# Kernel tuning notes

Hardware: AMD Instinct MI355X
Metric: run time of the kernel (lower is better)

Reference implementation:

```python
import jax, jax.numpy as jnp
import numpy as np

QUERY_DIM = 512
KEY_DIM = 512
HIDDEN_DIM = 512


def setup_inputs() -> dict:
    key = jax.random.key(0)
    k1, k2, k3, k4, k5 = jax.random.split(key, 5)
    B, S = 32, 2048
    query = jax.random.normal(k1, (B, QUERY_DIM), dtype=jnp.float32)
    keys = jax.random.normal(k2, (B, S, KEY_DIM), dtype=jnp.float32)
    # nn.Linear weights stored as [out_features, in_features]
    Wq = jax.random.normal(k3, (HIDDEN_DIM, QUERY_DIM), dtype=jnp.float32) / np.sqrt(QUERY_DIM)
    Wk = jax.random.normal(k4, (HIDDEN_DIM, KEY_DIM), dtype=jnp.float32) / np.sqrt(KEY_DIM)
    w_att = jax.random.normal(k5, (HIDDEN_DIM,), dtype=jnp.float32) / np.sqrt(HIDDEN_DIM)
    return {"query": query, "keys": keys, "Wq": Wq, "Wk": Wk, "w_att": w_att}


def reference(query, keys, Wq, Wk, w_att):
    # values defaults to keys
    values = keys
    q = query @ Wq.T                               # [B, H]
    k = jnp.einsum('bsd,hd->bsh', keys, Wk)        # [B, S, H]
    combined = jnp.tanh(q[:, None, :] + k)         # [B, S, H]
    scores = jnp.einsum('bsh,h->bs', combined, w_att)  # [B, S]
    attn = jax.nn.softmax(scores, axis=-1)         # [B, S]
    out = jnp.einsum('bs,bsd->bd', attn, values)   # [B, D]
    return (out, attn)
```

## Files before the change

kernel.cpp:

```cpp
#include <hip/hip_runtime.h>
#include <hip/hip_fp16.h>

typedef _Float16 f16x8 __attribute__((ext_vector_type(8)));
typedef float f32x4 __attribute__((ext_vector_type(4)));

#define WS_QV 0
#define WS_BF 65536
#define WS_SC 589824
#define WS_VP 851968

__global__ __launch_bounds__(256) void prep_kernel(
    const float* __restrict__ query, const float* __restrict__ Wq,
    const float* __restrict__ Wk, float* __restrict__ qv,
    _Float16* __restrict__ bfrag) {
  const int blk = blockIdx.x, tid = threadIdx.x;
  if (blk < 64) {
    const int b = blk >> 1;
    const int h = ((blk & 1) << 8) + tid;
    const float4* qr = (const float4*)(query + (size_t)b * 512);
    const float4* wr = (const float4*)(Wq + (size_t)h * 512);
    float acc = 0.f;
#pragma unroll 8
    for (int i = 0; i < 128; ++i) {
      float4 a = qr[i], w = wr[i];
      acc += a.x * w.x + a.y * w.y + a.z * w.z + a.w * w.w;
    }
    qv[b * 512 + h] = acc;
  } else {
    const int u = (blk - 64) * 4 + (tid >> 6);
    const int l = tid & 63;
    const int col = ((u >> 4) << 4) + (l & 15);
    const int k0 = ((u & 15) << 5) + ((l >> 4) << 3);
    const float4* src = (const float4*)(Wk + (size_t)col * 512 + k0);
    float4 x = src[0], y = src[1];
    f16x8 v;
    v[0] = (_Float16)x.x; v[1] = (_Float16)x.y;
    v[2] = (_Float16)x.z; v[3] = (_Float16)x.w;
    v[4] = (_Float16)y.x; v[5] = (_Float16)y.y;
    v[6] = (_Float16)y.z; v[7] = (_Float16)y.w;
    *(f16x8*)(bfrag + (size_t)u * 512 + l * 8) = v;
  }
}

__global__ __launch_bounds__(256, 2) void scores_kernel(
    const float* __restrict__ keys, const _Float16* __restrict__ bfrag,
    const float* __restrict__ qv, const float* __restrict__ w_att,
    float* __restrict__ scores) {
  __shared__ __align__(128) unsigned char lds[65536];
  const int tid = threadIdx.x, w = tid >> 6, l = tid & 63;
  const int wg = blockIdx.x;
  const int row0 = wg * 64;
  const int b = row0 >> 11;

  {
    const float* kb = keys + (size_t)row0 * 512;
#pragma unroll
    for (int j = 0; j < 16; ++j) {
      int u8 = j * 256 + tid;
      int r = u8 >> 6, c8 = u8 & 63;
      const float4* src = (const float4*)(kb + (size_t)r * 512 + c8 * 8);
      float4 x = src[0], y = src[1];
      f16x8 v;
      v[0] = (_Float16)x.x; v[1] = (_Float16)x.y;
      v[2] = (_Float16)x.z; v[3] = (_Float16)x.w;
      v[4] = (_Float16)y.x; v[5] = (_Float16)y.y;
      v[6] = (_Float16)y.z; v[7] = (_Float16)y.w;
      int byte = r * 1024 + c8 * 16;
      byte ^= (r & 7) << 4;
      *(f16x8*)(lds + byte) = v;
    }
  }
  __syncthreads();

  f32x4 acc[4][8];
#pragma unroll
  for (int mt = 0; mt < 4; ++mt)
#pragma unroll
    for (int nt = 0; nt < 8; ++nt) {
      acc[mt][nt][0] = 0.f; acc[mt][nt][1] = 0.f;
      acc[mt][nt][2] = 0.f; acc[mt][nt][3] = 0.f;
    }

  const int swz = (l & 7) << 4;
  const int acol = ((l >> 4) << 3) * 2;
  const int arow = (l & 15) * 1024;

#pragma unroll
  for (int kc = 0; kc < 8; ++kc) {
    f16x8 bf[8][2];
#pragma unroll
    for (int nt = 0; nt < 8; ++nt)
#pragma unroll
      for (int k2 = 0; k2 < 2; ++k2) {
        int u = (w * 8 + nt) * 16 + (kc * 2 + k2);
        bf[nt][k2] = *(const f16x8*)(bfrag + (size_t)u * 512 + l * 8);
      }
#pragma unroll
    for (int k2 = 0; k2 < 2; ++k2) {
      const int ks = kc * 2 + k2;
      f16x8 af[4];
#pragma unroll
      for (int mt = 0; mt < 4; ++mt) {
        int byte = (mt * 16384 + arow) + (ks * 64 + acol);
        byte ^= swz;
        af[mt] = *(const f16x8*)(lds + byte);
      }
#pragma unroll
      for (int mt = 0; mt < 4; ++mt)
#pragma unroll
        for (int nt = 0; nt < 8; ++nt)
          acc[mt][nt] = __builtin_amdgcn_mfma_f32_16x16x32_f16(
              af[mt], bf[nt][k2], acc[mt][nt], 0, 0, 0);
    }
  }

  float rs[16];
#pragma unroll
  for (int i = 0; i < 16; ++i) rs[i] = 0.f;
  const int hb = w * 128;
#pragma unroll
  for (int nt = 0; nt < 8; ++nt) {
    const int h = hb + nt * 16 + (l & 15);
    const float q = qv[b * 512 + h];
    const float wa = w_att[h];
#pragma unroll
    for (int mt = 0; mt < 4; ++mt)
#pragma unroll
      for (int r = 0; r < 4; ++r) {
        float x = q + acc[mt][nt][r];
        float e = __expf(x + x);
        float t = 1.f - __fdividef(2.f, e + 1.f);
        rs[mt * 4 + r] = __builtin_fmaf(t, wa, rs[mt * 4 + r]);
      }
  }
#pragma unroll
  for (int st = 1; st <= 8; st <<= 1)
#pragma unroll
    for (int i = 0; i < 16; ++i)
      rs[i] += __shfl_xor(rs[i], st, 64);

  __syncthreads();
  float* spart = (float*)lds;
  {
    const int idx = l & 15;
    float v = rs[0];
#pragma unroll
    for (int i = 1; i < 16; ++i) v = (idx == i) ? rs[i] : v;
    const int rrow = ((idx >> 2) << 4) + ((l >> 4) << 2) + (idx & 3);
    spart[w * 64 + rrow] = v;
  }
  __syncthreads();
  if (tid < 64) {
    float s = spart[tid] + spart[64 + tid] + spart[128 + tid] + spart[192 + tid];
    scores[row0 + tid] = s;
  }
}

__global__ __launch_bounds__(256) void out_kernel(
    const float* __restrict__ keys, const float* __restrict__ scores,
    float* __restrict__ attn_out, float* __restrict__ vpart) {
  __shared__ float red_mx[4], red_se[4];
  const int tid = threadIdx.x;
  const int b = blockIdx.x >> 5;
  const int sc = blockIdx.x & 31;
  const float* srow = scores + (size_t)b * 2048;

  float sv[8];
  float mx = -1e30f;
#pragma unroll
  for (int i = 0; i < 8; ++i) { sv[i] = srow[i * 256 + tid]; mx = fmaxf(mx, sv[i]); }
#pragma unroll
  for (int st = 32; st >= 1; st >>= 1) mx = fmaxf(mx, __shfl_xor(mx, st, 64));
  if ((tid & 63) == 0) red_mx[tid >> 6] = mx;
  __syncthreads();
  mx = fmaxf(fmaxf(red_mx[0], red_mx[1]), fmaxf(red_mx[2], red_mx[3]));

  float se = 0.f;
#pragma unroll
  for (int i = 0; i < 8; ++i) se += __expf(sv[i] - mx);
#pragma unroll
  for (int st = 32; st >= 1; st >>= 1) se += __shfl_xor(se, st, 64);
  if ((tid & 63) == 0) red_se[tid >> 6] = se;
  __syncthreads();
  se = red_se[0] + red_se[1] + red_se[2] + red_se[3];
  const float rinv = 1.f / se;

  if (tid < 64) {
    int s = sc * 64 + tid;
    attn_out[(size_t)b * 2048 + s] = __expf(srow[s] - mx) * rinv;
  }

  float acc0 = 0.f, acc1 = 0.f;
  const float* kb = keys + ((size_t)(b * 2048 + sc * 64)) * 512;
#pragma unroll 4
  for (int i = 0; i < 64; ++i) {
    float at = __expf(srow[sc * 64 + i] - mx) * rinv;
    acc0 = __builtin_fmaf(at, kb[(size_t)i * 512 + tid], acc0);
    acc1 = __builtin_fmaf(at, kb[(size_t)i * 512 + tid + 256], acc1);
  }
  vpart[(size_t)blockIdx.x * 512 + tid] = acc0;
  vpart[(size_t)blockIdx.x * 512 + tid + 256] = acc1;
}

__global__ __launch_bounds__(256) void reduce_kernel(
    const float* __restrict__ vpart, float* __restrict__ out) {
  const int t = blockIdx.x * 256 + threadIdx.x;
  const int b = t >> 9, d = t & 511;
  float s = 0.f;
#pragma unroll
  for (int sc = 0; sc < 32; ++sc)
    s += vpart[((size_t)(b * 32 + sc)) * 512 + d];
  out[t] = s;
}

extern "C" void kernel_launch(void* const* d_in, const int* in_sizes, int n_in,
                              void* d_out, int out_size, void* d_ws, size_t ws_size,
                              hipStream_t stream) {
  const float* query = (const float*)d_in[0];
  const float* keys  = (const float*)d_in[1];
  const float* Wq    = (const float*)d_in[2];
  const float* Wk    = (const float*)d_in[3];
  const float* w_att = (const float*)d_in[4];
  float* out  = (float*)d_out;
  float* attn = out + 16384;
  char* ws = (char*)d_ws;
  float*    qv     = (float*)(ws + WS_QV);
  _Float16* bfrag  = (_Float16*)(ws + WS_BF);
  float*    scores = (float*)(ws + WS_SC);
  float*    vpart  = (float*)(ws + WS_VP);

  prep_kernel<<<192, 256, 0, stream>>>(query, Wq, Wk, qv, bfrag);
  scores_kernel<<<1024, 256, 0, stream>>>(keys, bfrag, qv, w_att, scores);
  out_kernel<<<1024, 256, 0, stream>>>(keys, scores, attn, vpart);
  reduce_kernel<<<64, 256, 0, stream>>>(vpart, out);
}
```

Measured before the change: 108.4 us.

## Double-buffer K chunks in scores kernel and vectorize weighted-sum loads

The scores kernel now streams the 64-row keys tile in four 128-column chunks through a double-buffered 32KB LDS region. Each chunk's global loads sit in registers and overlap the MFMA work on the previous chunk, instead of staging the whole tile up front in 64KB of LDS. The smaller LDS footprint may also let more workgroups share a CU. In out_kernel, the weighted value sum uses float4 loads, with two row-halves combined through shared memory, which cuts load instruction count.

```diff
diff --git a/kernel.cpp b/kernel.cpp
--- a/kernel.cpp
+++ b/kernel.cpp
@@ -46,28 +46,30 @@
     const float* __restrict__ keys, const _Float16* __restrict__ bfrag,
     const float* __restrict__ qv, const float* __restrict__ w_att,
     float* __restrict__ scores) {
-  __shared__ __align__(128) unsigned char lds[65536];
+  __shared__ __align__(128) unsigned char lds[32768];
   const int tid = threadIdx.x, w = tid >> 6, l = tid & 63;
-  const int wg = blockIdx.x;
-  const int row0 = wg * 64;
+  const int row0 = blockIdx.x * 64;
   const int b = row0 >> 11;
 
+  const int sr = tid >> 2, scb = tid & 3;
+  const float* gsrc = keys + (size_t)(row0 + sr) * 512 + scb * 32;
+  const int wbase = sr * 256 + scb * 64;
+  const int wswz = (sr & 7) << 4;
+
+  float4 stg[8];
+#pragma unroll
+  for (int j = 0; j < 8; ++j) stg[j] = ((const float4*)gsrc)[j];
   {
-    const float* kb = keys + (size_t)row0 * 512;
-#pragma unroll
-    for (int j = 0; j < 16; ++j) {
-      int u8 = j * 256 + tid;
-      int r = u8 >> 6, c8 = u8 & 63;
-      const float4* src = (const float4*)(kb + (size_t)r * 512 + c8 * 8);
-      float4 x = src[0], y = src[1];
-      f16x8 v;
-      v[0] = (_Float16)x.x; v[1] = (_Float16)x.y;
-      v[2] = (_Float16)x.z; v[3] = (_Float16)x.w;
-      v[4] = (_Float16)y.x; v[5] = (_Float16)y.y;
-      v[6] = (_Float16)y.z; v[7] = (_Float16)y.w;
-      int byte = r * 1024 + c8 * 16;
-      byte ^= (r & 7) << 4;
-      *(f16x8*)(lds + byte) = v;
+    unsigned char* dbuf = lds;
+#pragma unroll
+    for (int j2 = 0; j2 < 4; ++j2) {
+      float4 x = stg[2 * j2], y = stg[2 * j2 + 1];
+      f16x8 h;
+      h[0] = (_Float16)x.x; h[1] = (_Float16)x.y;
+      h[2] = (_Float16)x.z; h[3] = (_Float16)x.w;
+      h[4] = (_Float16)y.x; h[5] = (_Float16)y.y;
+      h[6] = (_Float16)y.z; h[7] = (_Float16)y.w;
+      *(f16x8*)(dbuf + ((wbase + j2 * 16) ^ wswz)) = h;
     }
   }
   __syncthreads();
@@ -81,37 +83,58 @@
       acc[mt][nt][2] = 0.f; acc[mt][nt][3] = 0.f;
     }
 
-  const int swz = (l & 7) << 4;
-  const int acol = ((l >> 4) << 3) * 2;
-  const int arow = (l & 15) * 1024;
-
-#pragma unroll
-  for (int kc = 0; kc < 8; ++kc) {
-    f16x8 bf[8][2];
-#pragma unroll
-    for (int nt = 0; nt < 8; ++nt)
-#pragma unroll
-      for (int k2 = 0; k2 < 2; ++k2) {
-        int u = (w * 8 + nt) * 16 + (kc * 2 + k2);
-        bf[nt][k2] = *(const f16x8*)(bfrag + (size_t)u * 512 + l * 8);
-      }
-#pragma unroll
-    for (int k2 = 0; k2 < 2; ++k2) {
-      const int ks = kc * 2 + k2;
+  const int aswz = (l & 7) << 4;
+  const int arow = (l & 15) * 256;
+  const int acol = (l >> 4) << 4;
+
+#pragma unroll
+  for (int c = 0; c < 4; ++c) {
+    if (c < 3) {
+      const float4* g = (const float4*)(gsrc + (c + 1) * 128);
+#pragma unroll
+      for (int j = 0; j < 8; ++j) stg[j] = g[j];
+    }
+    __builtin_amdgcn_sched_barrier(0);
+
+    const unsigned char* buf = lds + (c & 1) * 16384;
+#pragma unroll
+    for (int kl = 0; kl < 4; ++kl) {
+      const int ks = c * 4 + kl;
+      f16x8 bf[8];
+#pragma unroll
+      for (int nt = 0; nt < 8; ++nt) {
+        int u = (w * 8 + nt) * 16 + ks;
+        bf[nt] = *(const f16x8*)(bfrag + (size_t)u * 512 + l * 8);
+      }
       f16x8 af[4];
 #pragma unroll
       for (int mt = 0; mt < 4; ++mt) {
-        int byte = (mt * 16384 + arow) + (ks * 64 + acol);
-        byte ^= swz;
-        af[mt] = *(const f16x8*)(lds + byte);
+        int byte = mt * 4096 + arow + ((kl * 64 + acol) ^ aswz);
+        af[mt] = *(const f16x8*)(buf + byte);
       }
 #pragma unroll
       for (int mt = 0; mt < 4; ++mt)
 #pragma unroll
         for (int nt = 0; nt < 8; ++nt)
           acc[mt][nt] = __builtin_amdgcn_mfma_f32_16x16x32_f16(
-              af[mt], bf[nt][k2], acc[mt][nt], 0, 0, 0);
-    }
+              af[mt], bf[nt], acc[mt][nt], 0, 0, 0);
+    }
+    __builtin_amdgcn_sched_barrier(0);
+
+    if (c < 3) {
+      unsigned char* dbuf = lds + ((c + 1) & 1) * 16384;
+#pragma unroll
+      for (int j2 = 0; j2 < 4; ++j2) {
+        float4 x = stg[2 * j2], y = stg[2 * j2 + 1];
+        f16x8 h;
+        h[0] = (_Float16)x.x; h[1] = (_Float16)x.y;
+        h[2] = (_Float16)x.z; h[3] = (_Float16)x.w;
+        h[4] = (_Float16)y.x; h[5] = (_Float16)y.y;
+        h[6] = (_Float16)y.z; h[7] = (_Float16)y.w;
+        *(f16x8*)(dbuf + ((wbase + j2 * 16) ^ wswz)) = h;
+      }
+    }
+    __syncthreads();
   }
 
   float rs[16];
@@ -160,6 +183,7 @@
     const float* __restrict__ keys, const float* __restrict__ scores,
     float* __restrict__ attn_out, float* __restrict__ vpart) {
   __shared__ float red_mx[4], red_se[4];
+  __shared__ float4 comb[128];
   const int tid = threadIdx.x;
   const int b = blockIdx.x >> 5;
   const int sc = blockIdx.x & 31;
@@ -190,16 +214,25 @@
     attn_out[(size_t)b * 2048 + s] = __expf(srow[s] - mx) * rinv;
   }
 
-  float acc0 = 0.f, acc1 = 0.f;
-  const float* kb = keys + ((size_t)(b * 2048 + sc * 64)) * 512;
+  const int c4 = tid & 127, rg = tid >> 7;
+  const float4* kb4 = (const float4*)(keys + ((size_t)(b * 2048 + sc * 64 + rg * 32)) * 512);
+  float4 a; a.x = 0.f; a.y = 0.f; a.z = 0.f; a.w = 0.f;
 #pragma unroll 4
-  for (int i = 0; i < 64; ++i) {
-    float at = __expf(srow[sc * 64 + i] - mx) * rinv;
-    acc0 = __builtin_fmaf(at, kb[(size_t)i * 512 + tid], acc0);
-    acc1 = __builtin_fmaf(at, kb[(size_t)i * 512 + tid + 256], acc1);
-  }
-  vpart[(size_t)blockIdx.x * 512 + tid] = acc0;
-  vpart[(size_t)blockIdx.x * 512 + tid + 256] = acc1;
+  for (int i = 0; i < 32; ++i) {
+    float at = __expf(srow[sc * 64 + rg * 32 + i] - mx) * rinv;
+    float4 kv = kb4[(size_t)i * 128 + c4];
+    a.x = __builtin_fmaf(at, kv.x, a.x);
+    a.y = __builtin_fmaf(at, kv.y, a.y);
+    a.z = __builtin_fmaf(at, kv.z, a.z);
+    a.w = __builtin_fmaf(at, kv.w, a.w);
+  }
+  if (rg) comb[c4] = a;
+  __syncthreads();
+  if (!rg) {
+    float4 o = comb[c4];
+    a.x += o.x; a.y += o.y; a.z += o.z; a.w += o.w;
+    ((float4*)vpart)[(size_t)blockIdx.x * 128 + c4] = a;
+  }
 }
 
 __global__ __launch_bounds__(256) void reduce_kernel(
```

After: 100.5 us. -7.3%, faster.
